# Kernel tuning notes

Hardware: AMD Instinct MI355X
Metric: run time of the kernel (lower is better)

## Reference

```python
import jax, jax.numpy as jnp
import numpy as np

ALIGNED_H = 7
ALIGNED_W = 7
SPATIAL_SCALE = 0.0625


def setup_inputs() -> dict:
    key = jax.random.key(0)
    k1, k2, k3, k4, k5, k6 = jax.random.split(key, 6)
    N, C, FH, FW = 4, 256, 100, 152
    R = 4000
    features = jax.random.normal(k1, (N, C, FH, FW), dtype=jnp.float32)
    x1 = jax.random.uniform(k2, (R,), minval=0.0, maxval=1800.0)
    y1 = jax.random.uniform(k3, (R,), minval=0.0, maxval=1200.0)
    bw = jax.random.uniform(k4, (R,), minval=16.0, maxval=400.0)
    bh = jax.random.uniform(k5, (R,), minval=16.0, maxval=300.0)
    rois = jnp.stack([x1, y1, x1 + bw, y1 + bh], axis=1).astype(jnp.float32)
    bids = jax.random.randint(k6, (R,), 0, N, dtype=jnp.int32)
    return {"features": features, "rois": rois, "bids": bids}


def _roi_align(features, rois, bids, AH, AW, scale):
    # features: [N,C,FH,FW]; rois: [R,4]; bids: [R] -> [R,C,AH,AW]
    N, C, FH, FW = features.shape
    r = rois * scale
    x1, y1, x2, y2 = r[:, 0], r[:, 1], r[:, 2], r[:, 3]
    bin_w = jnp.clip(x2 - x1 + 1.0, 0.0) / (AW - 1)
    bin_h = jnp.clip(y2 - y1 + 1.0, 0.0) / (AH - 1)
    h = y1[:, None] + jnp.arange(AH, dtype=features.dtype) * bin_h[:, None]  # [R,AH]
    w = x1[:, None] + jnp.arange(AW, dtype=features.dtype) * bin_w[:, None]  # [R,AW]
    valid_h = (h >= 0) & (h < FH)
    valid_w = (w >= 0) & (w < FW)
    hs = jnp.clip(jnp.floor(h), 0.0, FH - 2).astype(jnp.int32)  # [R,AH]
    ws = jnp.clip(jnp.floor(w), 0.0, FW - 2).astype(jnp.int32)  # [R,AW]
    hr = (h - hs)[:, :, None, None]  # [R,AH,1,1]
    wr = (w - ws)[:, None, :, None]  # [R,1,AW,1]
    b = bids[:, None, None]            # [R,1,1]
    hi = hs[:, :, None]                # [R,AH,1]
    wi = ws[:, None, :]                # [R,1,AW]
    def gather(dh, dw):
        # advanced indexing -> [R,AH,AW,C]
        return features[b, :, hi + dh, wi + dw]
    val = (gather(0, 0) * (1 - hr) * (1 - wr)
           + gather(0, 1) * (1 - hr) * wr
           + gather(1, 0) * hr * (1 - wr)
           + gather(1, 1) * hr * wr)
    mask = (valid_h[:, :, None] & valid_w[:, None, :])[:, :, :, None]
    val = jnp.where(mask, val, 0.0)
    return jnp.transpose(val, (0, 3, 1, 2))  # [R,C,AH,AW]


def reference(features, rois, bids):
    # RoIAlign on (aligned+1)^2 grid, then 2x2 stride-1 average pool -> 7x7
    x = _roi_align(features, rois, bids, ALIGNED_H + 1, ALIGNED_W + 1, SPATIAL_SCALE)
    out = (x[:, :, :-1, :-1] + x[:, :, :-1, 1:]
           + x[:, :, 1:, :-1] + x[:, :, 1:, 1:]) * 0.25
    return out
```

## Files before the change

### kernel.cpp

```cpp
#include <hip/hip_runtime.h>

#define N_IMG 4
#define C_CH  256
#define FH    100
#define FW    152
#define CHW   (C_CH * FH * FW)
#define OUT_PER_ROI (C_CH * 7 * 7)
#define SCALE 0.0625f
#define H_ROW_BYTES (FW * C_CH * 2)
#define H_CH_BYTES  (C_CH * 2)
#define CPAD 260

typedef float    f4 __attribute__((ext_vector_type(4)));
typedef _Float16 h4 __attribute__((ext_vector_type(4)));

__global__ __launch_bounds__(256) void bin_rois(
    const float* __restrict__ rois, const int* __restrict__ bids, int R,
    int* __restrict__ order) {
  __shared__ int hist[256];
  __shared__ int base[256];
  for (int k = threadIdx.x; k < 256; k += 256) hist[k] = 0;
  __syncthreads();
  for (int r = threadIdx.x; r < R; r += 256) {
    const float cx = (rois[r * 4 + 0] + rois[r * 4 + 2]) * 0.5f * SCALE;
    const float cy = (rois[r * 4 + 1] + rois[r * 4 + 3]) * 0.5f * SCALE;
    int xb = (int)(cx * (8.0f / FW)); xb = xb < 0 ? 0 : (xb > 7 ? 7 : xb);
    int yb = (int)(cy * (8.0f / FH)); yb = yb < 0 ? 0 : (yb > 7 ? 7 : yb);
    const int key = (bids[r] << 6) | (yb << 3) | xb;
    atomicAdd(&hist[key], 1);
  }
  __syncthreads();
  if (threadIdx.x == 0) {
    int s = 0;
    for (int k = 0; k < 256; ++k) { base[k] = s; s += hist[k]; }
  }
  __syncthreads();
  for (int r = threadIdx.x; r < R; r += 256) {
    const float cx = (rois[r * 4 + 0] + rois[r * 4 + 2]) * 0.5f * SCALE;
    const float cy = (rois[r * 4 + 1] + rois[r * 4 + 3]) * 0.5f * SCALE;
    int xb = (int)(cx * (8.0f / FW)); xb = xb < 0 ? 0 : (xb > 7 ? 7 : xb);
    int yb = (int)(cy * (8.0f / FH)); yb = yb < 0 ? 0 : (yb > 7 ? 7 : yb);
    const int key = (bids[r] << 6) | (yb << 3) | xb;
    const int pos = atomicAdd(&base[key], 1);
    order[pos] = r;
  }
}

__global__ __launch_bounds__(256) void transpose_nchw_nhwc(
    const float* __restrict__ in, _Float16* __restrict__ out) {
  const int x0 = blockIdx.x * 32;
  const int y  = blockIdx.y;
  const int b  = blockIdx.z;
  __shared__ float tile[32][C_CH + 4];
  const int chl = threadIdx.x & 31;
  const int xq  = threadIdx.x >> 5;
  const int x   = x0 + xq * 4;
  const bool inb = (x < FW);
  const float4* src4 = (const float4*)in;
#pragma unroll
  for (int cc = 0; cc < C_CH; cc += 32) {
    const int ch = cc + chl;
    float4 v = make_float4(0.f, 0.f, 0.f, 0.f);
    if (inb) v = src4[((size_t)b * C_CH + ch) * (FH * FW / 4) + y * (FW / 4) + (x >> 2)];
    tile[xq * 4 + 0][ch] = v.x;
    tile[xq * 4 + 1][ch] = v.y;
    tile[xq * 4 + 2][ch] = v.z;
    tile[xq * 4 + 3][ch] = v.w;
  }
  __syncthreads();
  const int chg = threadIdx.x & 63;
  const int xs  = threadIdx.x >> 6;
  _Float16* dstB = out + (((size_t)b * FH + y) * FW) * C_CH;
#pragma unroll
  for (int xi = 0; xi < 32; xi += 4) {
    const int xx = x0 + xi + xs;
    if (xx < FW) {
      const f4 v = *(const f4*)&tile[xi + xs][chg * 4];
      h4 hv;
      hv[0] = (_Float16)v[0]; hv[1] = (_Float16)v[1];
      hv[2] = (_Float16)v[2]; hv[3] = (_Float16)v[3];
      *(h4*)(dstB + (size_t)xx * C_CH + chg * 4) = hv;
    }
  }
}

__global__ __launch_bounds__(512, 4) void roialign_nhwc(
    const _Float16* __restrict__ feat, const float* __restrict__ rois,
    const int* __restrict__ bids, const int* __restrict__ order,
    int R, float* __restrict__ out) {
  const int g  = blockIdx.x;
  const int r  = order[((R & 7) == 0) ? ((g & 7) * (R >> 3) + (g >> 3)) : g];
  const int cg = threadIdx.x & 63;
  const int i  = threadIdx.x >> 6;
  __shared__ float smp[64 * CPAD];

  const float x1 = rois[r * 4 + 0] * SCALE;
  const float y1 = rois[r * 4 + 1] * SCALE;
  const float x2 = rois[r * 4 + 2] * SCALE;
  const float y2 = rois[r * 4 + 3] * SCALE;
  const int   b  = bids[r];
  const float bw = fmaxf(x2 - x1 + 1.0f, 0.0f) * (1.0f / 7.0f);
  const float bh = fmaxf(y2 - y1 + 1.0f, 0.0f) * (1.0f / 7.0f);

  const float h   = y1 + (float)i * bh;
  const float hsf = fminf(fmaxf(floorf(h), 0.0f), (float)(FH - 2));
  const float hr  = h - hsf;
  const float mh  = (h >= 0.0f && h < (float)FH) ? 1.0f : 0.0f;
  const float a0  = (1.0f - hr) * mh;
  const float a1  = hr * mh;

  const char* fbb  = (const char*)feat + (size_t)b * CHW * 2;
  const int   row0 = (int)hsf * H_ROW_BYTES + cg * 8;

  float* lbase = &smp[(i * 8) * CPAD + cg * 4];

#pragma unroll
  for (int j = 0; j < 8; ++j) {
    const float w   = x1 + (float)j * bw;
    const float wsf = fminf(fmaxf(floorf(w), 0.0f), (float)(FW - 2));
    const float wr  = w - wsf;
    const float mw  = (w >= 0.0f && w < (float)FW) ? 1.0f : 0.0f;
    const float q0  = (1.0f - wr) * mw;
    const float q1  = wr * mw;
    const int   o0  = row0 + (int)wsf * H_CH_BYTES;
    const h4 h00 = *(const h4*)(fbb + o0);
    const h4 h01 = *(const h4*)(fbb + o0 + H_CH_BYTES);
    const h4 h10 = *(const h4*)(fbb + o0 + H_ROW_BYTES);
    const h4 h11 = *(const h4*)(fbb + o0 + H_ROW_BYTES + H_CH_BYTES);
    const f4 g00 = __builtin_convertvector(h00, f4);
    const f4 g01 = __builtin_convertvector(h01, f4);
    const f4 g10 = __builtin_convertvector(h10, f4);
    const f4 g11 = __builtin_convertvector(h11, f4);
    const f4 s = (g00 * q0 + g01 * q1) * a0 + (g10 * q0 + g11 * q1) * a1;
    *(f4*)(lbase + j * CPAD) = s;
  }

  __syncthreads();

  f4* dst = (f4*)(out + (size_t)r * OUT_PER_ROI);
  const int g0 = (int)threadIdx.x * 4;
  int c   = (g0 * 669) >> 15;
  int rem = g0 - c * 49;
#pragma unroll
  for (int k = 0; k < 7; ++k) {
    const int idx = (int)threadIdx.x + k * 512;
    if (idx < (OUT_PER_ROI / 4)) {
      f4 v;
      int cc = c, rr = rem;
#pragma unroll
      for (int e = 0; e < 4; ++e) {
        const int p    = (rr * 37) >> 8;
        const int j    = rr - p * 7;
        const int base = (p * 8 + j) * CPAD + cc;
        v[e] = (smp[base] + smp[base + CPAD] +
                smp[base + 8 * CPAD] + smp[base + 9 * CPAD]) * 0.25f;
        if (++rr == 49) { rr = 0; ++cc; }
      }
      __builtin_nontemporal_store(v, dst + idx);
    }
    rem += 39; c += 41;
    if (rem >= 49) { rem -= 49; ++c; }
  }
}

extern "C" void kernel_launch(void* const* d_in, const int* in_sizes, int n_in,
                              void* d_out, int out_size, void* d_ws, size_t ws_size,
                              hipStream_t stream) {
  (void)n_in; (void)out_size; (void)ws_size;
  const float* features = (const float*)d_in[0];
  const float* rois     = (const float*)d_in[1];
  const int*   bids     = (const int*)d_in[2];
  float* out = (float*)d_out;
  const int R = in_sizes[1] / 4;

  _Float16* nhwc  = (_Float16*)d_ws;
  int*      order = (int*)((char*)d_ws + (64u << 20));

  bin_rois<<<1, 256, 0, stream>>>(rois, bids, R, order);
  dim3 tgrid((FW + 31) / 32, FH, N_IMG);
  transpose_nchw_nhwc<<<tgrid, 256, 0, stream>>>(features, nhwc);
  roialign_nhwc<<<R, 512, 0, stream>>>(nhwc, rois, bids, order, R, out);
}
```

Measured before the change: 285.8 us.

## Process two RoIs per block and prefetch second RoI's gathers during first's output

Each block now handles two RoIs: the feature gathers for the second RoI are issued into registers before the first RoI's shared-memory reduction and output store, so global load latency overlaps the write phase. The grid is halved and a custom barrier is used between phases. This raises register pressure (32 half4 loads held live) and may reduce occupancy under the 512x4 launch bound.

New measurement: 368.8 us. +29.0%, slower.

```diff
diff --git a/kernel.cpp b/kernel.cpp
--- a/kernel.cpp
+++ b/kernel.cpp
@@ -84,16 +84,15 @@
   }
 }
 
-__global__ __launch_bounds__(512, 4) void roialign_nhwc(
+struct RoiW {
+  float a0, a1;
+  float q0[8], q1[8];
+};
+
+__device__ __forceinline__ void roi_issue(
     const _Float16* __restrict__ feat, const float* __restrict__ rois,
-    const int* __restrict__ bids, const int* __restrict__ order,
-    int R, float* __restrict__ out) {
-  const int g  = blockIdx.x;
-  const int r  = order[((R & 7) == 0) ? ((g & 7) * (R >> 3) + (g >> 3)) : g];
-  const int cg = threadIdx.x & 63;
-  const int i  = threadIdx.x >> 6;
-  __shared__ float smp[64 * CPAD];
-
+    const int* __restrict__ bids, int r, int i, int cg,
+    RoiW& W, h4 ld[32]) {
   const float x1 = rois[r * 4 + 0] * SCALE;
   const float y1 = rois[r * 4 + 1] * SCALE;
   const float x2 = rois[r * 4 + 2] * SCALE;
@@ -101,49 +100,53 @@
   const int   b  = bids[r];
   const float bw = fmaxf(x2 - x1 + 1.0f, 0.0f) * (1.0f / 7.0f);
   const float bh = fmaxf(y2 - y1 + 1.0f, 0.0f) * (1.0f / 7.0f);
-
   const float h   = y1 + (float)i * bh;
   const float hsf = fminf(fmaxf(floorf(h), 0.0f), (float)(FH - 2));
   const float hr  = h - hsf;
   const float mh  = (h >= 0.0f && h < (float)FH) ? 1.0f : 0.0f;
-  const float a0  = (1.0f - hr) * mh;
-  const float a1  = hr * mh;
-
+  W.a0 = (1.0f - hr) * mh;
+  W.a1 = hr * mh;
   const char* fbb  = (const char*)feat + (size_t)b * CHW * 2;
   const int   row0 = (int)hsf * H_ROW_BYTES + cg * 8;
-
-  float* lbase = &smp[(i * 8) * CPAD + cg * 4];
-
 #pragma unroll
   for (int j = 0; j < 8; ++j) {
     const float w   = x1 + (float)j * bw;
     const float wsf = fminf(fmaxf(floorf(w), 0.0f), (float)(FW - 2));
     const float wr  = w - wsf;
     const float mw  = (w >= 0.0f && w < (float)FW) ? 1.0f : 0.0f;
-    const float q0  = (1.0f - wr) * mw;
-    const float q1  = wr * mw;
-    const int   o0  = row0 + (int)wsf * H_CH_BYTES;
-    const h4 h00 = *(const h4*)(fbb + o0);
-    const h4 h01 = *(const h4*)(fbb + o0 + H_CH_BYTES);
-    const h4 h10 = *(const h4*)(fbb + o0 + H_ROW_BYTES);
-    const h4 h11 = *(const h4*)(fbb + o0 + H_ROW_BYTES + H_CH_BYTES);
-    const f4 g00 = __builtin_convertvector(h00, f4);
-    const f4 g01 = __builtin_convertvector(h01, f4);
-    const f4 g10 = __builtin_convertvector(h10, f4);
-    const f4 g11 = __builtin_convertvector(h11, f4);
-    const f4 s = (g00 * q0 + g01 * q1) * a0 + (g10 * q0 + g11 * q1) * a1;
+    W.q0[j] = (1.0f - wr) * mw;
+    W.q1[j] = wr * mw;
+    const int o0 = row0 + (int)wsf * H_CH_BYTES;
+    ld[4 * j + 0] = *(const h4*)(fbb + o0);
+    ld[4 * j + 1] = *(const h4*)(fbb + o0 + H_CH_BYTES);
+    ld[4 * j + 2] = *(const h4*)(fbb + o0 + H_ROW_BYTES);
+    ld[4 * j + 3] = *(const h4*)(fbb + o0 + H_ROW_BYTES + H_CH_BYTES);
+  }
+}
+
+__device__ __forceinline__ void roi_compute_store(
+    const RoiW& W, const h4 ld[32], float* lbase) {
+#pragma unroll
+  for (int j = 0; j < 8; ++j) {
+    const f4 g00 = __builtin_convertvector(ld[4 * j + 0], f4);
+    const f4 g01 = __builtin_convertvector(ld[4 * j + 1], f4);
+    const f4 g10 = __builtin_convertvector(ld[4 * j + 2], f4);
+    const f4 g11 = __builtin_convertvector(ld[4 * j + 3], f4);
+    const f4 s = (g00 * W.q0[j] + g01 * W.q1[j]) * W.a0 +
+                 (g10 * W.q0[j] + g11 * W.q1[j]) * W.a1;
     *(f4*)(lbase + j * CPAD) = s;
   }
-
-  __syncthreads();
-
-  f4* dst = (f4*)(out + (size_t)r * OUT_PER_ROI);
-  const int g0 = (int)threadIdx.x * 4;
+}
+
+__device__ __forceinline__ void roi_phase2(
+    const float* __restrict__ smp, float* __restrict__ outr, int tid) {
+  f4* dst = (f4*)outr;
+  const int g0 = tid * 4;
   int c   = (g0 * 669) >> 15;
   int rem = g0 - c * 49;
 #pragma unroll
   for (int k = 0; k < 7; ++k) {
-    const int idx = (int)threadIdx.x + k * 512;
+    const int idx = tid + k * 512;
     if (idx < (OUT_PER_ROI / 4)) {
       f4 v;
       int cc = c, rr = rem;
@@ -163,6 +166,46 @@
   }
 }
 
+#define LDS_BARRIER()                                    \
+  do {                                                   \
+    asm volatile("s_waitcnt lgkmcnt(0)" ::: "memory");   \
+    __builtin_amdgcn_s_barrier();                        \
+  } while (0)
+
+__global__ __launch_bounds__(512, 4) void roialign_nhwc(
+    const _Float16* __restrict__ feat, const float* __restrict__ rois,
+    const int* __restrict__ bids, const int* __restrict__ order,
+    int R, float* __restrict__ out) {
+  const int nblk = (R + 1) >> 1;
+  const int g    = blockIdx.x;
+  const int swz  = ((nblk & 7) == 0) ? ((g & 7) * (nblk >> 3) + (g >> 3)) : g;
+  const bool hasB = (2 * swz + 1 < R);
+  const int rA   = order[2 * swz + 0];
+  const int rB   = hasB ? order[2 * swz + 1] : rA;
+  const int tid  = threadIdx.x;
+  const int cg   = tid & 63;
+  const int i    = tid >> 6;
+  __shared__ float smp[64 * CPAD];
+  float* lbase = &smp[(i * 8) * CPAD + cg * 4];
+
+  RoiW WA; h4 ldA[32];
+  roi_issue(feat, rois, bids, rA, i, cg, WA, ldA);
+  roi_compute_store(WA, ldA, lbase);
+
+  RoiW WB; h4 ldB[32];
+  if (hasB) roi_issue(feat, rois, bids, rB, i, cg, WB, ldB);
+
+  LDS_BARRIER();
+  roi_phase2(smp, out + (size_t)rA * OUT_PER_ROI, tid);
+
+  if (hasB) {
+    LDS_BARRIER();
+    roi_compute_store(WB, ldB, lbase);
+    LDS_BARRIER();
+    roi_phase2(smp, out + (size_t)rB * OUT_PER_ROI, tid);
+  }
+}
+
 extern "C" void kernel_launch(void* const* d_in, const int* in_sizes, int n_in,
                               void* d_out, int out_size, void* d_ws, size_t ws_size,
                               hipStream_t stream) {
@@ -179,5 +222,6 @@
   bin_rois<<<1, 256, 0, stream>>>(rois, bids, R, order);
   dim3 tgrid((FW + 31) / 32, FH, N_IMG);
   transpose_nchw_nhwc<<<tgrid, 256, 0, stream>>>(features, nhwc);
-  roialign_nhwc<<<R, 512, 0, stream>>>(nhwc, rois, bids, order, R, out);
-}
+  const int nblk = (R + 1) / 2;
+  roialign_nhwc<<<nblk, 512, 0, stream>>>(nhwc, rois, bids, order, R, out);
+}
```
